# Optimization experiments

Measured on AMD Instinct MI355X. Metric: run time of the kernel, lower is better.

## Reference

```python
import jax, jax.numpy as jnp
import numpy as np

EMBED_DIM = 1024
NUM_HEADS = 16
HEAD_DIM = EMBED_DIM // NUM_HEADS
B, S = 4, 2048


def setup_inputs() -> dict:
    key = jax.random.key(0)
    ks = jax.random.split(key, 9)
    scale = 1.0 / np.sqrt(EMBED_DIM)
    inp = {
        "inputs": jax.random.normal(ks[0], (B, S, EMBED_DIM), dtype=jnp.float32),
        "rotation_params": jax.random.normal(ks[1], (B, S, EMBED_DIM), dtype=jnp.float32),
        "entangle_params": jax.random.normal(ks[2], (B, S, EMBED_DIM), dtype=jnp.float32),
        # Linear weights stored as (out, in) like torch; applied as x @ W.T
        "Wq": jax.random.normal(ks[3], (EMBED_DIM, EMBED_DIM), dtype=jnp.float32) * scale,
        "Wk": jax.random.normal(ks[4], (EMBED_DIM, EMBED_DIM), dtype=jnp.float32) * scale,
        "Wv": jax.random.normal(ks[5], (EMBED_DIM, EMBED_DIM), dtype=jnp.float32) * scale,
        "Wrot": jax.random.normal(ks[6], (EMBED_DIM, EMBED_DIM), dtype=jnp.float32) * scale,
        "Went": jax.random.normal(ks[7], (EMBED_DIM, EMBED_DIM), dtype=jnp.float32) * scale,
        "Wo": jax.random.normal(ks[8], (EMBED_DIM, EMBED_DIM), dtype=jnp.float32) * scale,
    }
    return inp


def _split_heads(x):
    b, s, e = x.shape
    return x.reshape(b, s, NUM_HEADS, HEAD_DIM).transpose(0, 2, 1, 3)  # (B,H,S,D)


def reference(inputs, rotation_params, entangle_params, Wq, Wk, Wv, Wrot, Went, Wo):
    Q = inputs @ Wq.T + rotation_params @ Wrot.T
    K = inputs @ Wk.T + entangle_params @ Went.T
    V = inputs @ Wv.T
    Qh, Kh, Vh = _split_heads(Q), _split_heads(K), _split_heads(V)
    scores = jnp.einsum("bhqd,bhkd->bhqk", Qh, Kh) / jnp.sqrt(jnp.float32(HEAD_DIM))
    attn = jax.nn.softmax(scores, axis=-1)  # dropout p=0 -> identity
    out = jnp.einsum("bhqk,bhkd->bhqd", attn, Vh)
    out = out.transpose(0, 2, 1, 3).reshape(inputs.shape[0], inputs.shape[1], EMBED_DIM)
    return out @ Wo.T
```

## Files before the change

### kernel.cpp

```cpp
#include <hip/hip_runtime.h>
#include <stdint.h>


typedef unsigned short u16;
typedef __bf16 bf16x8 __attribute__((ext_vector_type(8)));
typedef float f32x4 __attribute__((ext_vector_type(4)));
typedef float f32x16 __attribute__((ext_vector_type(16)));
typedef uint32_t u32x4 __attribute__((ext_vector_type(4)));

#define MFMA_BF16(a, b, c) __builtin_amdgcn_mfma_f32_16x16x32_bf16((a), (b), (c), 0, 0, 0)
#define MFMA32(a, b, c)    __builtin_amdgcn_mfma_f32_32x32x16_bf16((a), (b), (c), 0, 0, 0)
#define GAMMA 0.18033688011112042f
#define BHSTRIDE 131072

static __device__ __forceinline__ u16 f2bf(float f) {
    uint32_t u = __builtin_bit_cast(uint32_t, f);
    u = (u + 0x7FFFu + ((u >> 16) & 1u)) >> 16;
    return (u16)u;
}

static __device__ __forceinline__ uint32_t pk_rne2(float a, float b) {
    uint32_t ua = __builtin_bit_cast(uint32_t, a);
    uint32_t ub = __builtin_bit_cast(uint32_t, b);
    ua += 0x7FFFu + ((ua >> 16) & 1u);
    ub += 0x7FFFu + ((ub >> 16) & 1u);
    return __builtin_amdgcn_perm(ub, ua, 0x07060302);
}

static __device__ __forceinline__ void async_copy16(const void* g, void* l) {
    __builtin_amdgcn_global_load_lds((__attribute__((address_space(1))) void*)g,
                                     (__attribute__((address_space(3))) void*)l,
                                     16, 0, 0);
}

static __device__ __forceinline__ uint32_t cvtpk(float a, float b) {
    uint32_t r;
    asm("v_cvt_pk_bf16_f32 %0, %1, %2" : "=v"(r) : "v"(a), "v"(b));
    return r;
}

static __device__ __forceinline__ void plswap(uint32_t& a, uint32_t& b) {
    asm("v_permlane32_swap_b32 %0, %1" : "+v"(a), "+v"(b));
}

static __device__ __forceinline__ bf16x8 mkfrag(uint32_t w0, uint32_t w1,
                                                uint32_t w2, uint32_t w3) {
    u32x4 u = {w0, w1, w2, w3};
    return __builtin_bit_cast(bf16x8, u);
}

struct CvtArgs { const float* s[6]; u16* d[6]; };

__global__ __launch_bounds__(256) void cvt_kernel(CvtArgs a, int nelem) {
    const float* s = a.s[blockIdx.z];
    u16* d = a.d[blockIdx.z];
    int i = (blockIdx.x * 256 + threadIdx.x) * 8;
    float4 f0 = *(const float4*)(s + i);
    float4 f1 = *(const float4*)(s + i + 4);
    uint4 w;
    w.x = pk_rne2(f0.x, f0.y); w.y = pk_rne2(f0.z, f0.w);
    w.z = pk_rne2(f1.x, f1.y); w.w = pk_rne2(f1.z, f1.w);
    *(uint4*)(d + i) = w;
}

template <int AMODE, int CMODE>
__global__ __launch_bounds__(256, 2) void gemm_bt(
    const u16* __restrict__ A0, const u16* __restrict__ W0,
    const u16* __restrict__ A1, const u16* __restrict__ W1,
    void* __restrict__ Cv, int K, int npairs, float scale)
{
    __shared__ __align__(16) u16 lA[128 * 32];
    __shared__ __align__(16) u16 lB[128 * 32];

    const int tid  = threadIdx.x;
    const int lane = tid & 63;
    const int wave = tid >> 6;
    const int wm   = (wave >> 1) * 64;
    const int wn   = (wave & 1) * 64;
    const size_t m0 = (size_t)blockIdx.x * 128;
    const size_t n0 = (size_t)blockIdx.y * 128;

    const int r  = tid >> 2;
    const int c8 = (tid & 3) * 8;
    const int fr = lane & 15;
    const int g  = lane >> 4;

    const size_t bb = (m0 >> 11) * 16;
    const size_t s0 = m0 & 2047;

    f32x4 acc[4][4] = {};

    for (int p = 0; p < npairs; ++p) {
        const u16* A = p ? A1 : A0;
        const u16* W = p ? W1 : W0;
        for (int k0 = 0; k0 < K; k0 += 32) {
            __syncthreads();
            if (AMODE == 0) {
                async_copy16(A + ((m0 + r) * (size_t)K + k0 + c8),      lA + tid * 8);
                async_copy16(A + ((m0 + r + 64) * (size_t)K + k0 + c8), lA + 2048 + tid * 8);
            } else {
                int ch = k0 + c8;
                size_t base = (bb + (size_t)(ch >> 6)) * BHSTRIDE + (ch & 63);
                async_copy16(A + base + (s0 + r) * 64,      lA + tid * 8);
                async_copy16(A + base + (s0 + r + 64) * 64, lA + 2048 + tid * 8);
            }
            async_copy16(W + ((n0 + r) * (size_t)K + k0 + c8),      lB + tid * 8);
            async_copy16(W + ((n0 + r + 64) * (size_t)K + k0 + c8), lB + 2048 + tid * 8);
            __syncthreads();

            bf16x8 af[4], bf[4];
#pragma unroll
            for (int i = 0; i < 4; ++i)
                af[i] = *(const bf16x8*)(lA + (wm + i * 16 + fr) * 32 + g * 8);
#pragma unroll
            for (int i = 0; i < 4; ++i)
                bf[i] = *(const bf16x8*)(lB + (wn + i * 16 + fr) * 32 + g * 8);
#pragma unroll
            for (int i = 0; i < 4; ++i)
#pragma unroll
                for (int j = 0; j < 4; ++j)
                    acc[i][j] = MFMA_BF16(af[i], bf[j], acc[i][j]);
        }
    }

#pragma unroll
    for (int i = 0; i < 4; ++i)
#pragma unroll
        for (int j = 0; j < 4; ++j) {
            if (CMODE == 2) {
                size_t row0 = m0 + wm + i * 16 + g * 4;
                size_t col  = n0 + wn + j * 16 + fr;
                size_t addr = ((row0 >> 11) * 16 + (col >> 6)) * BHSTRIDE
                            + (size_t)(col & 63) * 2048 + (row0 & 2047);
                ushort4 pk;
                pk.x = f2bf(acc[i][j][0] * scale);
                pk.y = f2bf(acc[i][j][1] * scale);
                pk.z = f2bf(acc[i][j][2] * scale);
                pk.w = f2bf(acc[i][j][3] * scale);
                *(ushort4*)((u16*)Cv + addr) = pk;
            } else {
#pragma unroll
                for (int rg = 0; rg < 4; ++rg) {
                    size_t row = m0 + wm + i * 16 + g * 4 + rg;
                    size_t col = n0 + wn + j * 16 + fr;
                    float v = acc[i][j][rg] * scale;
                    if (CMODE == 0) {
                        ((float*)Cv)[row * 1024 + col] = v;
                    } else {
                        size_t addr = ((row >> 11) * 16 + (col >> 6)) * BHSTRIDE
                                    + (row & 2047) * 64 + (col & 63);
                        ((u16*)Cv)[addr] = f2bf(v);
                    }
                }
            }
        }
}

__global__ __launch_bounds__(256, 2) void flash_kernel(
    const u16* __restrict__ Qhm, const u16* __restrict__ Khm,
    const u16* __restrict__ Vt, u16* __restrict__ Ohm)
{
    __shared__ __align__(16) u16 sK[2][128 * 64];
    __shared__ __align__(16) u16 sVt[2][64 * 128];

    const int tid  = threadIdx.x;
    const int lane = tid & 63;
    const int wave = tid >> 6;
    const int l31  = lane & 31;
    const int hg   = lane >> 5;

    const int lin  = blockIdx.x;
    const int slot = lin >> 3;
    const int bh   = (lin & 7) + 8 * (slot >> 3);
    const int q0   = (slot & 7) * 256;

    const u16* Qh = Qhm + (size_t)bh * BHSTRIDE;
    const u16* Kh = Khm + (size_t)bh * BHSTRIDE;
    const u16* Vh = Vt  + (size_t)bh * BHSTRIDE;
    u16*       Oh = Ohm + (size_t)bh * BHSTRIDE;

    bf16x8 qbf[2][4];
#pragma unroll
    for (int qt = 0; qt < 2; ++qt)
#pragma unroll
        for (int dc = 0; dc < 4; ++dc)
            qbf[qt][dc] = *(const bf16x8*)(Qh +
                (size_t)(q0 + wave * 64 + qt * 32 + l31) * 64 + dc * 16 + hg * 8);

    f32x16 oacc[2][2] = {};
    float lsum[2] = {};

    const int krow8 = tid >> 3, kcp = tid & 7;
    const int vd16  = tid >> 4, vcp = tid & 15;

    auto stage = [&](int buf, int kt) {
#pragma unroll
        for (int it = 0; it < 4; ++it) {
            int row = it * 32 + krow8;
            int sc = kcp ^ (((row >> 3) ^ row) & 7);
            async_copy16(Kh + (size_t)(kt * 128 + row) * 64 + sc * 8,
                         (char*)(&sK[buf][0]) + it * 4096 + tid * 16);
        }
#pragma unroll
        for (int it = 0; it < 4; ++it) {
            int d = it * 16 + vd16;
            int sc = vcp ^ (d & 15);
            async_copy16(Vh + (size_t)d * 2048 + kt * 128 + sc * 8,
                         (char*)(&sVt[buf][0]) + it * 4096 + tid * 16);
        }
    };

    stage(0, 0);
    __syncthreads();

    int cur = 0;
    for (int kt = 0; kt < 16; ++kt) {
        if (kt < 15) stage(cur ^ 1, kt + 1);
        const u16* sKc = &sK[cur][0];
        const u16* sVc = &sVt[cur][0];

#pragma unroll
        for (int kc = 0; kc < 4; ++kc) {
            f32x16 sa0 = {}, sa1 = {};
            const int krow = kc * 32 + l31;
            const int ksw = ((krow >> 3) ^ krow) & 7;
#pragma unroll
            for (int dc = 0; dc < 4; ++dc) {
                bf16x8 ka = *(const bf16x8*)(sKc + krow * 64 + ((dc * 2 + hg) ^ ksw) * 8);
                sa0 = MFMA32(ka, qbf[0][dc], sa0);
                sa1 = MFMA32(ka, qbf[1][dc], sa1);
            }
            bf16x8 vb[2][2];
#pragma unroll
            for (int sub = 0; sub < 2; ++sub)
#pragma unroll
                for (int dt = 0; dt < 2; ++dt) {
                    int dr = dt * 32 + l31;
                    vb[sub][dt] = *(const bf16x8*)(sVc + dr * 128 +
                        ((kc * 4 + sub * 2 + hg) ^ (dr & 15)) * 8);
                }
#pragma unroll
            for (int qt = 0; qt < 2; ++qt) {
                const f32x16 sa = qt ? sa1 : sa0;
                float p[16];
#pragma unroll
                for (int r = 0; r < 16; ++r) {
                    p[r] = exp2f(sa[r]);
                    lsum[qt] += p[r];
                }
                uint32_t w0 = cvtpk(p[0],  p[1]),  w1 = cvtpk(p[2],  p[3]);
                uint32_t w2 = cvtpk(p[4],  p[5]),  w3 = cvtpk(p[6],  p[7]);
                uint32_t w4 = cvtpk(p[8],  p[9]),  w5 = cvtpk(p[10], p[11]);
                uint32_t w6 = cvtpk(p[12], p[13]), w7 = cvtpk(p[14], p[15]);
                plswap(w0, w2); plswap(w1, w3);
                plswap(w4, w6); plswap(w5, w7);
                bf16x8 pa0 = mkfrag(w0, w1, w2, w3);
                bf16x8 pa1 = mkfrag(w4, w5, w6, w7);
                oacc[qt][0] = MFMA32(pa0, vb[0][0], oacc[qt][0]);
                oacc[qt][1] = MFMA32(pa0, vb[0][1], oacc[qt][1]);
                oacc[qt][0] = MFMA32(pa1, vb[1][0], oacc[qt][0]);
                oacc[qt][1] = MFMA32(pa1, vb[1][1], oacc[qt][1]);
            }
        }
        __syncthreads();
        cur ^= 1;
    }

#pragma unroll
    for (int qt = 0; qt < 2; ++qt) {
        float l = lsum[qt];
        l += __shfl_xor(l, 32);
        float inv = 1.0f / l;
#pragma unroll
        for (int r = 0; r < 16; ++r) {
            int row = (r & 3) + 4 * hg + 8 * (r >> 2);
            float invr = __shfl(inv, row);
            size_t grow = (size_t)q0 + wave * 64 + qt * 32 + row;
            Oh[grow * 64 + l31]      = f2bf(oacc[qt][0][r] * invr);
            Oh[grow * 64 + 32 + l31] = f2bf(oacc[qt][1][r] * invr);
        }
    }
}

extern "C" void kernel_launch(void* const* d_in, const int* in_sizes, int n_in,
                              void* d_out, int out_size, void* d_ws, size_t ws_size,
                              hipStream_t stream)
{
    const float* X    = (const float*)d_in[0];
    const float* R    = (const float*)d_in[1];
    const float* E    = (const float*)d_in[2];
    const float* Wq   = (const float*)d_in[3];
    const float* Wk   = (const float*)d_in[4];
    const float* Wv   = (const float*)d_in[5];
    const float* Wrot = (const float*)d_in[6];
    const float* Went = (const float*)d_in[7];
    const float* Wo   = (const float*)d_in[8];

    const size_t NT = 8192 * 1024;
    const size_t NW = 1024 * 1024;

    u16* Qhm = (u16*)d_out;
    u16* Khm = Qhm + NT;
    u16* Xb  = (u16*)d_ws;
    u16* RVb = Xb + NT;
    u16* EOb = RVb + NT;
    u16* Wqb = EOb + NT;
    u16* Wkb   = Wqb + NW;
    u16* Wvb   = Wkb + NW;
    u16* Wrotb = Wvb + NW;
    u16* Wentb = Wrotb + NW;
    u16* Wob   = Wentb + NW;

    {
        CvtArgs a{};
        a.s[0] = X; a.s[1] = R; a.s[2] = E;
        a.d[0] = Xb; a.d[1] = RVb; a.d[2] = EOb;
        cvt_kernel<<<dim3(4096, 1, 3), 256, 0, stream>>>(a, (int)NT);
    }
    {
        CvtArgs a{};
        a.s[0] = Wq; a.s[1] = Wk; a.s[2] = Wv; a.s[3] = Wrot; a.s[4] = Went; a.s[5] = Wo;
        a.d[0] = Wqb; a.d[1] = Wkb; a.d[2] = Wvb; a.d[3] = Wrotb; a.d[4] = Wentb; a.d[5] = Wob;
        cvt_kernel<<<dim3(512, 1, 6), 256, 0, stream>>>(a, (int)NW);
    }

    dim3 gproj(64, 8);
    gemm_bt<0, 1><<<gproj, 256, 0, stream>>>(Xb, Wqb, RVb, Wrotb, Qhm, 1024, 2, GAMMA);
    gemm_bt<0, 1><<<gproj, 256, 0, stream>>>(Xb, Wkb, EOb, Wentb, Khm, 1024, 2, 1.0f);
    gemm_bt<0, 2><<<gproj, 256, 0, stream>>>(Xb, Wvb, nullptr, nullptr, RVb, 1024, 1, 1.0f);
    flash_kernel<<<dim3(512), 256, 0, stream>>>(Qhm, Khm, RVb, EOb);
    gemm_bt<1, 0><<<gproj, 256, 0, stream>>>(EOb, Wob, nullptr, nullptr, d_out, 1024, 1, 1.0f);
}
```

Before: 406.0 us.

## Widen GEMM K-tile to 64 with swizzled LDS and shrink flash tiles

The projection GEMM now stages 64-wide K slices with an XOR-swizzled LDS layout, which halves the number of barrier-separated iterations and avoids bank conflicts on fragment reads. The flash attention kernel is reworked so each block handles 128 queries (32 per wave) with 64-key tiles. The grid doubles to 1024 blocks and the launch bound rises to allow 4 blocks per CU. This trades per-wave reuse of K/V tiles for higher occupancy and more parallelism, at the cost of more K/V reloads overall and more loop iterations.

```diff
diff --git a/kernel.cpp b/kernel.cpp
--- a/kernel.cpp
+++ b/kernel.cpp
@@ -69,8 +69,8 @@
     const u16* __restrict__ A1, const u16* __restrict__ W1,
     void* __restrict__ Cv, int K, int npairs, float scale)
 {
-    __shared__ __align__(16) u16 lA[128 * 32];
-    __shared__ __align__(16) u16 lB[128 * 32];
+    __shared__ __align__(16) u16 lA[128 * 64];
+    __shared__ __align__(16) u16 lB[128 * 64];
 
     const int tid  = threadIdx.x;
     const int lane = tid & 63;
@@ -80,10 +80,10 @@
     const size_t m0 = (size_t)blockIdx.x * 128;
     const size_t n0 = (size_t)blockIdx.y * 128;
 
-    const int r  = tid >> 2;
-    const int c8 = (tid & 3) * 8;
-    const int fr = lane & 15;
-    const int g  = lane >> 4;
+    const int row8 = tid >> 3;
+    const int cp   = tid & 7;
+    const int fr   = lane & 15;
+    const int g    = lane >> 4;
 
     const size_t bb = (m0 >> 11) * 16;
     const size_t s0 = m0 & 2047;
@@ -93,33 +93,47 @@
     for (int p = 0; p < npairs; ++p) {
         const u16* A = p ? A1 : A0;
         const u16* W = p ? W1 : W0;
-        for (int k0 = 0; k0 < K; k0 += 32) {
+        for (int k0 = 0; k0 < K; k0 += 64) {
             __syncthreads();
-            if (AMODE == 0) {
-                async_copy16(A + ((m0 + r) * (size_t)K + k0 + c8),      lA + tid * 8);
-                async_copy16(A + ((m0 + r + 64) * (size_t)K + k0 + c8), lA + 2048 + tid * 8);
-            } else {
-                int ch = k0 + c8;
-                size_t base = (bb + (size_t)(ch >> 6)) * BHSTRIDE + (ch & 63);
-                async_copy16(A + base + (s0 + r) * 64,      lA + tid * 8);
-                async_copy16(A + base + (s0 + r + 64) * 64, lA + 2048 + tid * 8);
-            }
-            async_copy16(W + ((n0 + r) * (size_t)K + k0 + c8),      lB + tid * 8);
-            async_copy16(W + ((n0 + r + 64) * (size_t)K + k0 + c8), lB + 2048 + tid * 8);
+#pragma unroll
+            for (int it = 0; it < 4; ++it) {
+                int row = it * 32 + row8;
+                int sc = cp ^ (((row >> 3) ^ row) & 7);
+                if (AMODE == 0) {
+                    async_copy16(A + ((m0 + row) * (size_t)K + k0 + sc * 8),
+                                 (char*)lA + it * 4096 + tid * 16);
+                } else {
+                    size_t base = (bb + (size_t)(k0 >> 6)) * BHSTRIDE;
+                    async_copy16(A + base + (s0 + row) * 64 + sc * 8,
+                                 (char*)lA + it * 4096 + tid * 16);
+                }
+                async_copy16(W + ((n0 + row) * (size_t)K + k0 + sc * 8),
+                             (char*)lB + it * 4096 + tid * 16);
+            }
             __syncthreads();
 
-            bf16x8 af[4], bf[4];
+            bf16x8 af[4][2], bfm[4][2];
+#pragma unroll
+            for (int i = 0; i < 4; ++i) {
+                int row = wm + i * 16 + fr;
+                int sw = ((row >> 3) ^ row) & 7;
+                af[i][0] = *(const bf16x8*)(lA + row * 64 + (g ^ sw) * 8);
+                af[i][1] = *(const bf16x8*)(lA + row * 64 + ((4 + g) ^ sw) * 8);
+            }
+#pragma unroll
+            for (int j = 0; j < 4; ++j) {
+                int row = wn + j * 16 + fr;
+                int sw = ((row >> 3) ^ row) & 7;
+                bfm[j][0] = *(const bf16x8*)(lB + row * 64 + (g ^ sw) * 8);
+                bfm[j][1] = *(const bf16x8*)(lB + row * 64 + ((4 + g) ^ sw) * 8);
+            }
 #pragma unroll
             for (int i = 0; i < 4; ++i)
-                af[i] = *(const bf16x8*)(lA + (wm + i * 16 + fr) * 32 + g * 8);
-#pragma unroll
-            for (int i = 0; i < 4; ++i)
-                bf[i] = *(const bf16x8*)(lB + (wn + i * 16 + fr) * 32 + g * 8);
-#pragma unroll
-            for (int i = 0; i < 4; ++i)
-#pragma unroll
-                for (int j = 0; j < 4; ++j)
-                    acc[i][j] = MFMA_BF16(af[i], bf[j], acc[i][j]);
+#pragma unroll
+                for (int j = 0; j < 4; ++j) {
+                    acc[i][j] = MFMA_BF16(af[i][0], bfm[j][0], acc[i][j]);
+                    acc[i][j] = MFMA_BF16(af[i][1], bfm[j][1], acc[i][j]);
+                }
         }
     }
 
@@ -156,12 +170,12 @@
         }
 }
 
-__global__ __launch_bounds__(256, 2) void flash_kernel(
+__global__ __launch_bounds__(256, 4) void flash_kernel(
     const u16* __restrict__ Qhm, const u16* __restrict__ Khm,
     const u16* __restrict__ Vt, u16* __restrict__ Ohm)
 {
-    __shared__ __align__(16) u16 sK[2][128 * 64];
-    __shared__ __align__(16) u16 sVt[2][64 * 128];
+    __shared__ __align__(16) u16 sK[2][64 * 64];
+    __shared__ __align__(16) u16 sVt[2][64 * 64];
 
     const int tid  = threadIdx.x;
     const int lane = tid & 63;
@@ -171,41 +185,38 @@
 
     const int lin  = blockIdx.x;
     const int slot = lin >> 3;
-    const int bh   = (lin & 7) + 8 * (slot >> 3);
-    const int q0   = (slot & 7) * 256;
+    const int bh   = (lin & 7) + 8 * (slot >> 4);
+    const int q0   = (slot & 15) * 128;
 
     const u16* Qh = Qhm + (size_t)bh * BHSTRIDE;
     const u16* Kh = Khm + (size_t)bh * BHSTRIDE;
     const u16* Vh = Vt  + (size_t)bh * BHSTRIDE;
     u16*       Oh = Ohm + (size_t)bh * BHSTRIDE;
 
-    bf16x8 qbf[2][4];
-#pragma unroll
-    for (int qt = 0; qt < 2; ++qt)
-#pragma unroll
-        for (int dc = 0; dc < 4; ++dc)
-            qbf[qt][dc] = *(const bf16x8*)(Qh +
-                (size_t)(q0 + wave * 64 + qt * 32 + l31) * 64 + dc * 16 + hg * 8);
-
-    f32x16 oacc[2][2] = {};
-    float lsum[2] = {};
-
-    const int krow8 = tid >> 3, kcp = tid & 7;
-    const int vd16  = tid >> 4, vcp = tid & 15;
+    bf16x8 qbf[4];
+#pragma unroll
+    for (int dc = 0; dc < 4; ++dc)
+        qbf[dc] = *(const bf16x8*)(Qh +
+            (size_t)(q0 + wave * 32 + l31) * 64 + dc * 16 + hg * 8);
+
+    f32x16 oacc[2] = {};
+    float lsum = 0.0f;
+
+    const int row8 = tid >> 3, cp = tid & 7;
 
     auto stage = [&](int buf, int kt) {
 #pragma unroll
-        for (int it = 0; it < 4; ++it) {
-            int row = it * 32 + krow8;
-            int sc = kcp ^ (((row >> 3) ^ row) & 7);
-            async_copy16(Kh + (size_t)(kt * 128 + row) * 64 + sc * 8,
+        for (int it = 0; it < 2; ++it) {
+            int row = it * 32 + row8;
+            int sc = cp ^ (((row >> 3) ^ row) & 7);
+            async_copy16(Kh + (size_t)(kt * 64 + row) * 64 + sc * 8,
                          (char*)(&sK[buf][0]) + it * 4096 + tid * 16);
         }
 #pragma unroll
-        for (int it = 0; it < 4; ++it) {
-            int d = it * 16 + vd16;
-            int sc = vcp ^ (d & 15);
-            async_copy16(Vh + (size_t)d * 2048 + kt * 128 + sc * 8,
+        for (int it = 0; it < 2; ++it) {
+            int d = it * 32 + row8;
+            int sc = cp ^ (d & 7);
+            async_copy16(Vh + (size_t)d * 2048 + kt * 64 + sc * 8,
                          (char*)(&sVt[buf][0]) + it * 4096 + tid * 16);
         }
     };
@@ -214,21 +225,20 @@
     __syncthreads();
 
     int cur = 0;
-    for (int kt = 0; kt < 16; ++kt) {
-        if (kt < 15) stage(cur ^ 1, kt + 1);
+    for (int kt = 0; kt < 32; ++kt) {
+        if (kt < 31) stage(cur ^ 1, kt + 1);
         const u16* sKc = &sK[cur][0];
         const u16* sVc = &sVt[cur][0];
 
 #pragma unroll
-        for (int kc = 0; kc < 4; ++kc) {
-            f32x16 sa0 = {}, sa1 = {};
+        for (int kc = 0; kc < 2; ++kc) {
+            f32x16 sa = {};
             const int krow = kc * 32 + l31;
             const int ksw = ((krow >> 3) ^ krow) & 7;
 #pragma unroll
             for (int dc = 0; dc < 4; ++dc) {
                 bf16x8 ka = *(const bf16x8*)(sKc + krow * 64 + ((dc * 2 + hg) ^ ksw) * 8);
-                sa0 = MFMA32(ka, qbf[0][dc], sa0);
-                sa1 = MFMA32(ka, qbf[1][dc], sa1);
+                sa = MFMA32(ka, qbf[dc], sa);
             }
             bf16x8 vb[2][2];
 #pragma unroll
@@ -236,48 +246,43 @@
 #pragma unroll
                 for (int dt = 0; dt < 2; ++dt) {
                     int dr = dt * 32 + l31;
-                    vb[sub][dt] = *(const bf16x8*)(sVc + dr * 128 +
-                        ((kc * 4 + sub * 2 + hg) ^ (dr & 15)) * 8);
+                    vb[sub][dt] = *(const bf16x8*)(sVc + dr * 64 +
+                        ((kc * 4 + sub * 2 + hg) ^ (dr & 7)) * 8);
                 }
-#pragma unroll
-            for (int qt = 0; qt < 2; ++qt) {
-                const f32x16 sa = qt ? sa1 : sa0;
-                float p[16];
-#pragma unroll
-                for (int r = 0; r < 16; ++r) {
-                    p[r] = exp2f(sa[r]);
-                    lsum[qt] += p[r];
-                }
-                uint32_t w0 = cvtpk(p[0],  p[1]),  w1 = cvtpk(p[2],  p[3]);
-                uint32_t w2 = cvtpk(p[4],  p[5]),  w3 = cvtpk(p[6],  p[7]);
-                uint32_t w4 = cvtpk(p[8],  p[9]),  w5 = cvtpk(p[10], p[11]);
-                uint32_t w6 = cvtpk(p[12], p[13]), w7 = cvtpk(p[14], p[15]);
-                plswap(w0, w2); plswap(w1, w3);
-                plswap(w4, w6); plswap(w5, w7);
-                bf16x8 pa0 = mkfrag(w0, w1, w2, w3);
-                bf16x8 pa1 = mkfrag(w4, w5, w6, w7);
-                oacc[qt][0] = MFMA32(pa0, vb[0][0], oacc[qt][0]);
-                oacc[qt][1] = MFMA32(pa0, vb[0][1], oacc[qt][1]);
-                oacc[qt][0] = MFMA32(pa1, vb[1][0], oacc[qt][0]);
-                oacc[qt][1] = MFMA32(pa1, vb[1][1], oacc[qt][1]);
-            }
+            float p[16];
+#pragma unroll
+            for (int r = 0; r < 16; ++r) {
+                p[r] = exp2f(sa[r]);
+                lsum += p[r];
+            }
+            uint32_t w0 = cvtpk(p[0],  p[1]),  w1 = cvtpk(p[2],  p[3]);
+            uint32_t w2 = cvtpk(p[4],  p[5]),  w3 = cvtpk(p[6],  p[7]);
+            uint32_t w4 = cvtpk(p[8],  p[9]),  w5 = cvtpk(p[10], p[11]);
+            uint32_t w6 = cvtpk(p[12], p[13]), w7 = cvtpk(p[14], p[15]);
+            plswap(w0, w2); plswap(w1, w3);
+            plswap(w4, w6); plswap(w5, w7);
+            bf16x8 pa0 = mkfrag(w0, w1, w2, w3);
+            bf16x8 pa1 = mkfrag(w4, w5, w6, w7);
+            oacc[0] = MFMA32(pa0, vb[0][0], oacc[0]);
+            oacc[1] = MFMA32(pa0, vb[0][1], oacc[1]);
+            oacc[0] = MFMA32(pa1, vb[1][0], oacc[0]);
+            oacc[1] = MFMA32(pa1, vb[1][1], oacc[1]);
         }
         __syncthreads();
         cur ^= 1;
     }
 
-#pragma unroll
-    for (int qt = 0; qt < 2; ++qt) {
-        float l = lsum[qt];
+    {
+        float l = lsum;
         l += __shfl_xor(l, 32);
         float inv = 1.0f / l;
 #pragma unroll
         for (int r = 0; r < 16; ++r) {
             int row = (r & 3) + 4 * hg + 8 * (r >> 2);
             float invr = __shfl(inv, row);
-            size_t grow = (size_t)q0 + wave * 64 + qt * 32 + row;
-            Oh[grow * 64 + l31]      = f2bf(oacc[qt][0][r] * invr);
-            Oh[grow * 64 + 32 + l31] = f2bf(oacc[qt][1][r] * invr);
+            size_t grow = (size_t)q0 + wave * 32 + row;
+            Oh[grow * 64 + l31]      = f2bf(oacc[0][r] * invr);
+            Oh[grow * 64 + 32 + l31] = f2bf(oacc[1][r] * invr);
         }
     }
 }
@@ -328,6 +333,6 @@
     gemm_bt<0, 1><<<gproj, 256, 0, stream>>>(Xb, Wqb, RVb, Wrotb, Qhm, 1024, 2, GAMMA);
     gemm_bt<0, 1><<<gproj, 256, 0, stream>>>(Xb, Wkb, EOb, Wentb, Khm, 1024, 2, 1.0f);
     gemm_bt<0, 2><<<gproj, 256, 0, stream>>>(Xb, Wvb, nullptr, nullptr, RVb, 1024, 1, 1.0f);
-    flash_kernel<<<dim3(512), 256, 0, stream>>>(Qhm, Khm, RVb, EOb);
+    flash_kernel<<<dim3(1024), 256, 0, stream>>>(Qhm, Khm, RVb, EOb);
     gemm_bt<1, 0><<<gproj, 256, 0, stream>>>(EOb, Wob, nullptr, nullptr, d_out, 1024, 1, 1.0f);
 }
```

Result: faster. 391.9 us (-3.5%).
